# Performance work log

Hardware: AMD Instinct MI355X
Metric: run time of the kernel (lower is better)

Reference implementation:

```python
import jax, jax.numpy as jnp
import numpy as np
from jax import lax

BS, T, H, V, E, NREG, SEQ = 1024, 10, 256, 50000, 50, 1, 50
EPS = 1e-5


def _edge_index(bs):
    # get_batch_graph(max_len=10, windows=3): per graph, edges[0:-1] of combinations keeps
    # (j-3, j-2) and (j-3, j-1) for j in 3..10, plus (8,9) and (9,0). 18 edges/graph.
    e = []
    for j in range(3, 11):
        e += [(j - 3, j - 2), (j - 3, j - 1)]
    e += [(8, 9), (9, 0)]
    e = np.asarray(e, dtype=np.int32)                      # [18, 2]
    e = (e[None] + 10 * np.arange(bs, dtype=np.int32)[:, None, None]).reshape(-1, 2)
    return jnp.asarray(e[:, 0]), jnp.asarray(e[:, 1])      # src, dst


def setup_inputs() -> dict:
    key = jax.random.key(0)
    ks = jax.random.split(key, 24)
    s = 0.02
    inp = {
        'lags': jax.random.normal(ks[0], (BS, T), jnp.float32),
        'weather': jax.random.normal(ks[1], (BS, T, 2), jnp.float32),
        'event': jax.random.normal(ks[2], (BS, T, 4), jnp.float32),
        'text': jax.random.randint(ks[3], (BS, T, SEQ), 0, V, jnp.int32),
        'emb': jax.random.normal(ks[4], (V, E), jnp.float32) * s,
        'conv3_w': jax.random.normal(ks[5], (H // 2, E, 3), jnp.float32) * s,
        'conv3_b': jnp.zeros((H // 2,), jnp.float32),
        'conv4_w': jax.random.normal(ks[6], (H // 2, H // 2, 4), jnp.float32) * s,
        'conv4_b': jnp.zeros((H // 2,), jnp.float32),
        'lags_w': jax.random.normal(ks[7], (H, 1), jnp.float32) * s,
        'lags_b': jnp.zeros((H,), jnp.float32),
        'weather_w': jax.random.normal(ks[8], (H, 2), jnp.float32) * s,
        'weather_b': jnp.zeros((H,), jnp.float32),
        'event_w': jax.random.normal(ks[9], (H, 4), jnp.float32) * s,
        'event_b': jnp.zeros((H,), jnp.float32),
        'text_w': jax.random.normal(ks[10], (H, H // 2), jnp.float32) * s,
        'text_b': jnp.zeros((H,), jnp.float32),
        'merge_w': jax.random.normal(ks[11], (H, 4 * H), jnp.float32) * s,
        'merge_b': jnp.zeros((H,), jnp.float32),
        'bn_gamma': jnp.ones((H,), jnp.float32),
        'bn_beta': jnp.zeros((H,), jnp.float32),
        'mh_w': jax.random.normal(ks[12], (H, H), jnp.float32) * s,
        'mh_b': jnp.zeros((H,), jnp.float32),
        'gru_wih': jax.random.normal(ks[13], (3 * H, H), jnp.float32) * s,
        'gru_whh': jax.random.normal(ks[14], (3 * H, H), jnp.float32) * s,
        'gru_bih': jnp.zeros((3 * H,), jnp.float32),
        'gru_bhh': jnp.zeros((3 * H,), jnp.float32),
        'reg_w': jax.random.normal(ks[15], (NREG, T * H), jnp.float32) * s,
        'reg_b': jnp.zeros((NREG,), jnp.float32),
    }
    return inp


def _conv1d(x, w, b):
    # x: [N, Cin, L], w: [Cout, Cin, K] (torch layout)
    y = lax.conv_general_dilated(x, w, (1,), 'VALID',
                                 dimension_numbers=('NCH', 'OIH', 'NCH'))
    return y + b[None, :, None]


def _forward(lags, weather, event, text, emb, conv3_w, conv3_b, conv4_w, conv4_b,
             lags_w, lags_b, weather_w, weather_b, event_w, event_b, text_w, text_b,
             merge_w, merge_b, bn_gamma, bn_beta, mh_w, mh_b,
             gru_wih, gru_whh, gru_bih, gru_bhh, reg_w, reg_b):
    bs = lags.shape[0]
    n = bs * T
    h = mh_w.shape[0]

    # per-node feature projections
    l = lags.reshape(-1, 1) @ lags_w.T + lags_b                       # [N, H]
    w = weather.reshape(-1, 2) @ weather_w.T + weather_b              # [N, H]
    ev = event.reshape(-1, 4) @ event_w.T + event_b                   # [N, H]

    # text CNN branch (dropout = identity, eval mode)
    tx = emb[text.reshape(-1, SEQ)]                                   # [N, 50, E]
    tx = jnp.transpose(tx, (0, 2, 1))                                 # [N, E, 50]
    c3 = jax.nn.relu(_conv1d(tx, conv3_w, conv3_b))                   # [N, H/2, 48]
    c4 = jax.nn.relu(_conv1d(c3, conv4_w, conv4_b))                   # [N, H/2, 45]
    tx = jnp.max(c4, axis=2)                                          # [N, H/2]
    tx = tx @ text_w.T + text_b                                       # [N, H]

    # message passing: sum mailbox per destination node (all nodes have in-deg >= 1)
    src, dst = _edge_index(bs)
    def agg(f):
        return jax.ops.segment_sum(f[src], dst, num_segments=n)
    hcat = jnp.concatenate([agg(l), agg(w), agg(ev), agg(tx)], axis=-1)  # [N, 4H]

    # fused linear -> relu -> batchnorm (batch stats) -> linear
    m = jax.nn.relu(hcat @ merge_w.T + merge_b)
    mu = jnp.mean(m, axis=0)
    var = jnp.var(m, axis=0)
    m = (m - mu) / jnp.sqrt(var + EPS) * bn_gamma + bn_beta
    m = m @ mh_w.T + mh_b                                             # [N, H]

    # GRU over the 10 lag steps
    hg = m.reshape(bs, T, h)
    def step(hprev, x_t):
        gi = x_t @ gru_wih.T + gru_bih
        gh = hprev @ gru_whh.T + gru_bhh
        r = jax.nn.sigmoid(gi[:, :h] + gh[:, :h])
        z = jax.nn.sigmoid(gi[:, h:2 * h] + gh[:, h:2 * h])
        nn_ = jnp.tanh(gi[:, 2 * h:] + r * gh[:, 2 * h:])
        hnew = (1.0 - z) * nn_ + z * hprev
        return hnew, hnew
    h0 = jnp.zeros((bs, h), m.dtype)
    _, outs = lax.scan(step, h0, jnp.transpose(hg, (1, 0, 2)))        # [T, bs, H]
    out = jnp.transpose(outs, (1, 0, 2)).reshape(bs, -1)              # [bs, T*H]
    return out @ reg_w.T + reg_b                                      # [bs, n_reg]


def reference(lags, weather, event, text, emb, conv3_w, conv3_b, conv4_w, conv4_b,
              lags_w, lags_b, weather_w, weather_b, event_w, event_b, text_w, text_b,
              merge_w, merge_b, bn_gamma, bn_beta, mh_w, mh_b,
              gru_wih, gru_whh, gru_bih, gru_bhh, reg_w, reg_b):
    return _forward(lags, weather, event, text, emb, conv3_w, conv3_b, conv4_w, conv4_b,
                    lags_w, lags_b, weather_w, weather_b, event_w, event_b, text_w, text_b,
                    merge_w, merge_b, bn_gamma, bn_beta, mh_w, mh_b,
                    gru_wih, gru_whh, gru_bih, gru_bhh, reg_w, reg_b)
```

## Files before the change

### kernel.cpp

```cpp
#include <hip/hip_runtime.h>
#include <math.h>


typedef unsigned short u16;
typedef __attribute__((ext_vector_type(8))) short short8v;
typedef __attribute__((ext_vector_type(4))) float float4v;
#define MFMA16 __builtin_amdgcn_mfma_f32_16x16x32_bf16

__device__ inline u16 f2bf(float f) {
  unsigned u = __float_as_uint(f);
  u += 0x7FFFu + ((u >> 16) & 1u);
  return (u16)(u >> 16);
}

__global__ __launch_bounds__(256) void k_zero(float* __restrict__ p, int n) {
  int i = blockIdx.x * 256 + threadIdx.x;
  if (i < n) p[i] = 0.f;
}

__global__ __launch_bounds__(256) void k_repb3(const float* __restrict__ w3,
                                               u16* __restrict__ w3b) {
  int i = blockIdx.x * 256 + threadIdx.x;
  if (i >= 24576) return;
  int j = i & 7, l = (i >> 3) & 63, nt = (i >> 9) & 7, kt = i >> 12;
  int k = kt * 32 + (l >> 4) * 8 + j;
  int c = nt * 16 + (l & 15);
  int kk = k >> 6, e = k & 63;
  float v = (e < 50) ? w3[c * 150 + e * 3 + kk] : 0.f;
  w3b[i] = f2bf(v);
}

__global__ __launch_bounds__(256) void k_repb4(const float* __restrict__ w4,
                                               u16* __restrict__ w4b) {
  int i = blockIdx.x * 256 + threadIdx.x;
  int j = i & 7, l = (i >> 3) & 63, nt = (i >> 9) & 7, kt = i >> 12;
  int k = kt * 32 + (l >> 4) * 8 + j;
  int c = nt * 16 + (l & 15);
  int kk = k >> 7, ci = k & 127;
  w4b[i] = f2bf(w4[c * 512 + ci * 4 + kk]);
}

__global__ __launch_bounds__(256) void k_repwhh(const float* __restrict__ whh,
                                                u16* __restrict__ whhb) {
  int i = blockIdx.x * 256 + threadIdx.x;
  int j = i & 7, l = (i >> 3) & 63, kt = (i >> 9) & 7, nt = i >> 12;
  int n = nt * 16 + (l & 15);
  int k = kt * 32 + (l >> 4) * 8 + j;
  whhb[i] = f2bf(whh[n * 256 + k]);
}

__global__ __launch_bounds__(256) void k_pcomb(const float* __restrict__ wih,
                                               const float* __restrict__ mh_w,
                                               const float* __restrict__ mh_b,
                                               const float* __restrict__ bih,
                                               float* __restrict__ Wcomb,
                                               float* __restrict__ b1) {
  int g0 = blockIdx.x * 8, t = threadIdx.x;
  float acc[8] = {0.f, 0.f, 0.f, 0.f, 0.f, 0.f, 0.f, 0.f};
  for (int j = 0; j < 256; ++j) {
    float wv = mh_w[j * 256 + t];
#pragma unroll
    for (int r = 0; r < 8; ++r) acc[r] += wih[(g0 + r) * 256 + j] * wv;
  }
#pragma unroll
  for (int r = 0; r < 8; ++r) Wcomb[(g0 + r) * 256 + t] = acc[r];
  __shared__ float red[4][8];
  float mb = mh_b[t];
#pragma unroll
  for (int r = 0; r < 8; ++r) {
    float v = wih[(g0 + r) * 256 + t] * mb;
    v += __shfl_down(v, 32); v += __shfl_down(v, 16); v += __shfl_down(v, 8);
    v += __shfl_down(v, 4);  v += __shfl_down(v, 2);  v += __shfl_down(v, 1);
    if ((t & 63) == 0) red[t >> 6][r] = v;
  }
  __syncthreads();
  if (t < 8) b1[g0 + t] = bih[g0 + t] + red[0][t] + red[1][t] + red[2][t] + red[3][t];
}

__global__ __launch_bounds__(256) void k_pmerge(const float* __restrict__ merge_w,
                                                const float* __restrict__ text_w,
                                                const float* __restrict__ lags_w,
                                                const float* __restrict__ weather_w,
                                                const float* __restrict__ event_w,
                                                const float* __restrict__ lags_b,
                                                const float* __restrict__ weather_b,
                                                const float* __restrict__ event_b,
                                                const float* __restrict__ text_b,
                                                float* __restrict__ MtxT,
                                                float* __restrict__ A_l,
                                                float* __restrict__ MwT,
                                                float* __restrict__ MeT,
                                                float* __restrict__ bias_deg) {
  int blk = blockIdx.x, t = threadIdx.x;
  if (blk < 128) {
    int c = blk;
    float acc = 0.f;
    for (int j = 0; j < 256; ++j)
      acc += merge_w[t * 1024 + 768 + j] * text_w[j * 128 + c];
    MtxT[c * 256 + t] = acc;
  } else {
    float a = 0.f, w0 = 0.f, w1 = 0.f, e0 = 0.f, e1 = 0.f, e2 = 0.f, e3 = 0.f, bd = 0.f;
    for (int j = 0; j < 256; ++j) {
      float m0 = merge_w[t * 1024 + j];
      float m1 = merge_w[t * 1024 + 256 + j];
      float m2 = merge_w[t * 1024 + 512 + j];
      float m3 = merge_w[t * 1024 + 768 + j];
      a  += m0 * lags_w[j];
      w0 += m1 * weather_w[j * 2 + 0];
      w1 += m1 * weather_w[j * 2 + 1];
      e0 += m2 * event_w[j * 4 + 0];
      e1 += m2 * event_w[j * 4 + 1];
      e2 += m2 * event_w[j * 4 + 2];
      e3 += m2 * event_w[j * 4 + 3];
      bd += m0 * lags_b[j] + m1 * weather_b[j] + m2 * event_b[j] + m3 * text_b[j];
    }
    A_l[t] = a;
    MwT[t] = w0; MwT[256 + t] = w1;
    MeT[t] = e0; MeT[256 + t] = e1; MeT[512 + t] = e2; MeT[768 + t] = e3;
    bias_deg[t] = bd;
  }
}


#define LOADB4(DST, SRC, KT)                                                   \
  _Pragma("unroll") for (int q = 0; q < 4; ++q)                                \
      DST[q] = *(const short8v*)&SRC[((((KT) * 8 + NB + q) * 64) + l) * 8];

#define AFRAG3(AF, KT) {                                                       \
    const int kk_ = (KT) >> 1;                                                 \
    const int eb_ = 4 * ((KT) & 1) + g;                                        \
    _Pragma("unroll") for (int mt = 0; mt < 3; ++mt) {                         \
      int pr_ = 16 * mt + lr + kk_;                                            \
      int bb_ = eb_ ^ (pr_ & 7);                                               \
      AF[mt] = *(const short8v*)&sx[pr_ * 64 + bb_ * 8];                       \
    } }

#define AFRAG4(AF, KT) {                                                       \
    const int t4_ = 4 * (KT) + g;                                              \
    const int kk_ = t4_ >> 4;                                                  \
    const int bk_ = t4_ & 15;                                                  \
    _Pragma("unroll") for (int mt = 0; mt < 3; ++mt) {                         \
      int pr_ = 16 * mt + lr + kk_;                                            \
      int bb_ = (bk_ & 8) | ((bk_ ^ pr_) & 7);                                 \
      AF[mt] = *(const short8v*)&sc3[pr_ * 128 + bb_ * 8];                     \
    } }

#define MSTEP4(AF, BF)                                                         \
  _Pragma("unroll") for (int q = 0; q < 4; ++q)                                \
    _Pragma("unroll") for (int mt = 0; mt < 3; ++mt)                           \
      acc[mt][q] = MFMA16(AF[mt], BF[q], acc[mt][q], 0, 0, 0);

__global__ __launch_bounds__(128) void k_textcnn(const int* __restrict__ text,
                                                 const float* __restrict__ emb,
                                                 const u16* __restrict__ w3b,
                                                 const float* __restrict__ b3,
                                                 const u16* __restrict__ w4b,
                                                 const float* __restrict__ b4,
                                                 float* __restrict__ mx_g) {
  __shared__ u16 sbuf[52 * 128];
  u16* sx = sbuf;
  u16* sc3 = sbuf;
  const int n = blockIdx.x;
  const int t = threadIdx.x;
  const int wv = t >> 6;
  const int l = t & 63;
  const int lr = l & 15;
  const int g = l >> 4;
  const int NB = wv * 4;

  int idxv = (l < 25) ? text[n * 50 + wv * 25 + l] : 0;
  const int e = l;
#pragma unroll 5
  for (int si = 0; si < 25; ++si) {
    int s = wv * 25 + si;
    int id = __shfl(idxv, si);
    float v = (e < 50) ? emb[id * 50 + e] : 0.f;
    int bb = (e >> 3) ^ (s & 7);
    sx[s * 64 + bb * 8 + (e & 7)] = f2bf(v);
  }
  __syncthreads();

  const float4v zv = {0.f, 0.f, 0.f, 0.f};
  float4v acc[3][4];
#pragma unroll
  for (int mt = 0; mt < 3; ++mt)
#pragma unroll
    for (int q = 0; q < 4; ++q) acc[mt][q] = zv;

  float b3v[4];
#pragma unroll
  for (int q = 0; q < 4; ++q) b3v[q] = b3[(NB + q) * 16 + lr];

  {
    short8v bA[4], bB[4], a[3];
    LOADB4(bA, w3b, 0);
    for (int kt = 0; kt < 6; kt += 2) {
      LOADB4(bB, w3b, kt + 1);
      AFRAG3(a, kt);
      MSTEP4(a, bA);
      if (kt + 2 < 6) LOADB4(bA, w3b, kt + 2);
      AFRAG3(a, kt + 1);
      MSTEP4(a, bB);
    }
  }
  __syncthreads();

#pragma unroll
  for (int mt = 0; mt < 3; ++mt)
#pragma unroll
    for (int q = 0; q < 4; ++q) {
#pragma unroll
      for (int r = 0; r < 4; ++r) {
        int p = 16 * mt + 4 * g + r;
        int c = (NB + q) * 16 + lr;
        float v = fmaxf(acc[mt][q][r] + b3v[q], 0.f);
        int bb = (c >> 3) & 15;
        bb = (bb & 8) | ((bb ^ (p & 7)) & 7);
        sc3[p * 128 + bb * 8 + (c & 7)] = f2bf(v);
      }
      acc[mt][q] = zv;
    }
  __syncthreads();

  {
    short8v bA[4], bB[4], a[3];
    LOADB4(bA, w4b, 0);
    for (int kt = 0; kt < 16; kt += 2) {
      LOADB4(bB, w4b, kt + 1);
      AFRAG4(a, kt);
      MSTEP4(a, bA);
      if (kt + 2 < 16) LOADB4(bA, w4b, kt + 2);
      AFRAG4(a, kt + 1);
      MSTEP4(a, bB);
    }
  }

#pragma unroll
  for (int q = 0; q < 4; ++q) {
    float m0 = -1e30f;
#pragma unroll
    for (int mt = 0; mt < 3; ++mt)
#pragma unroll
      for (int r = 0; r < 4; ++r) {
        int p = 16 * mt + 4 * g + r;
        if (p < 45) m0 = fmaxf(m0, acc[mt][q][r]);
      }
    m0 = fmaxf(m0, __shfl_xor(m0, 16));
    m0 = fmaxf(m0, __shfl_xor(m0, 32));
    int c = (NB + q) * 16 + lr;
    float bias = b4[c];
    if (g == 0) mx_g[n * 128 + c] = fmaxf(m0 + bias, 0.f);
  }
}

__device__ inline void preds_of(int i, int& p1, int& p2, int& d) {
  int tt = i % 10;
  int base = i - tt;
  if (tt == 0)      { p1 = base + 9;      p2 = -1;             d = 1; }
  else if (tt == 1) { p1 = base;          p2 = -1;             d = 1; }
  else              { p1 = base + tt - 2; p2 = base + tt - 1;  d = 2; }
}

__global__ __launch_bounds__(256) void k_merge(const float* __restrict__ mx_g,
                                               const float* __restrict__ lags,
                                               const float* __restrict__ weather,
                                               const float* __restrict__ event,
                                               const float* __restrict__ MtxT,
                                               const float* __restrict__ A_l,
                                               const float* __restrict__ MwT,
                                               const float* __restrict__ MeT,
                                               const float* __restrict__ bias_deg,
                                               const float* __restrict__ merge_b,
                                               u16* __restrict__ m_bf,
                                               float* __restrict__ bnsum,
                                               float* __restrict__ bnsumsq) {
  __shared__ __align__(16) float mxs[16 * 128];
  __shared__ float scal[16 * 8];
  const int tid = threadIdx.x;
  const int row0 = blockIdx.x * 16;
  for (int idx = tid; idx < 2048; idx += 256) {
    int r = idx >> 7, c = idx & 127;
    int p1, p2, d;
    preds_of(row0 + r, p1, p2, d);
    float v = mx_g[p1 * 128 + c];
    if (p2 >= 0) v += mx_g[p2 * 128 + c];
    mxs[r * 128 + c] = v;
  }
  if (tid < 16) {
    int p1, p2, d;
    preds_of(row0 + tid, p1, p2, d);
    float sl = lags[p1];
    float sw0 = weather[p1 * 2], sw1 = weather[p1 * 2 + 1];
    float se0 = event[p1 * 4], se1 = event[p1 * 4 + 1];
    float se2 = event[p1 * 4 + 2], se3 = event[p1 * 4 + 3];
    if (p2 >= 0) {
      sl += lags[p2];
      sw0 += weather[p2 * 2]; sw1 += weather[p2 * 2 + 1];
      se0 += event[p2 * 4];     se1 += event[p2 * 4 + 1];
      se2 += event[p2 * 4 + 2]; se3 += event[p2 * 4 + 3];
    }
    scal[tid * 8 + 0] = sl;
    scal[tid * 8 + 1] = sw0; scal[tid * 8 + 2] = sw1;
    scal[tid * 8 + 3] = se0; scal[tid * 8 + 4] = se1;
    scal[tid * 8 + 5] = se2; scal[tid * 8 + 6] = se3;
    scal[tid * 8 + 7] = (float)d;
  }
  __syncthreads();
  const int t = tid;
  float acc[16];
#pragma unroll
  for (int r = 0; r < 16; ++r) acc[r] = 0.f;
  for (int c4 = 0; c4 < 32; ++c4) {
    const int c = c4 * 4;
    float w0 = MtxT[c * 256 + t];
    float w1 = MtxT[(c + 1) * 256 + t];
    float w2 = MtxT[(c + 2) * 256 + t];
    float w3 = MtxT[(c + 3) * 256 + t];
#pragma unroll
    for (int r = 0; r < 16; ++r) {
      float4 mv = *(const float4*)&mxs[r * 128 + c];
      acc[r] += mv.x * w0 + mv.y * w1 + mv.z * w2 + mv.w * w3;
    }
  }
  float al = A_l[t], mw0 = MwT[t], mw1 = MwT[256 + t];
  float me0 = MeT[t], me1 = MeT[256 + t], me2 = MeT[512 + t], me3 = MeT[768 + t];
  float bd = bias_deg[t], mb = merge_b[t];
  float s1 = 0.f, s2 = 0.f;
#pragma unroll
  for (int r = 0; r < 16; ++r) {
    float mp = acc[r] + scal[r * 8] * al + scal[r * 8 + 1] * mw0 + scal[r * 8 + 2] * mw1
             + scal[r * 8 + 3] * me0 + scal[r * 8 + 4] * me1 + scal[r * 8 + 5] * me2
             + scal[r * 8 + 6] * me3 + scal[r * 8 + 7] * bd + mb;
    float mv = fmaxf(mp, 0.f);
    m_bf[(row0 + r) * 256 + t] = f2bf(mv);
    s1 += mv;
    s2 += mv * mv;
  }
  atomicAdd(&bnsum[t], s1);
  atomicAdd(&bnsumsq[t], s2);
}

__global__ __launch_bounds__(256) void k_bna(const float* __restrict__ bnsum,
                                             const float* __restrict__ bnsumsq,
                                             const float* __restrict__ gamma,
                                             const float* __restrict__ beta,
                                             float* __restrict__ svec,
                                             float* __restrict__ tvec) {
  int c = threadIdx.x;
  float mu = bnsum[c] * (1.f / 10240.f);
  float var = bnsumsq[c] * (1.f / 10240.f) - mu * mu;
  float s = gamma[c] * rsqrtf(var + 1e-5f);
  svec[c] = s;
  tvec[c] = beta[c] - mu * s;
}

__global__ __launch_bounds__(256) void k_bnbc(const float* __restrict__ Wcomb,
                                              const float* __restrict__ svec,
                                              const float* __restrict__ tvec,
                                              const float* __restrict__ b1,
                                              u16* __restrict__ wbig_b,
                                              float* __restrict__ bias_big) {
  int blk = blockIdx.x, t = threadIdx.x;
  __shared__ float red[4];
  if (blk < 768) {
    int i = blk * 256 + t;
    int j = i & 7, l = (i >> 3) & 63, kt = (i >> 9) & 7, nt = i >> 12;
    int n = nt * 16 + (l & 15);
    int k = kt * 32 + (l >> 4) * 8 + j;
    wbig_b[i] = f2bf(Wcomb[n * 256 + k] * svec[k]);
  } else {
    int gg = blk - 768;
    float part = tvec[t] * Wcomb[gg * 256 + t];
    part += __shfl_down(part, 32); part += __shfl_down(part, 16);
    part += __shfl_down(part, 8);  part += __shfl_down(part, 4);
    part += __shfl_down(part, 2);  part += __shfl_down(part, 1);
    if ((t & 63) == 0) red[t >> 6] = part;
    __syncthreads();
    if (t == 0) bias_big[gg] = b1[gg] + red[0] + red[1] + red[2] + red[3];
  }
}

__global__ __launch_bounds__(256) void k_gi(const u16* __restrict__ m_bf,
                                            const u16* __restrict__ wbig_b,
                                            const float* __restrict__ bias_big,
                                            float* __restrict__ gi) {
  const int t = threadIdx.x;
  const int w = t >> 6, l = t & 63, lr = l & 15, g = l >> 4;
  const int row0 = blockIdx.x * 16;
  short8v a[8];
#pragma unroll
  for (int kt = 0; kt < 8; ++kt)
    a[kt] = *(const short8v*)&m_bf[(row0 + lr) * 256 + kt * 32 + g * 8];
  const float4v zv = {0.f, 0.f, 0.f, 0.f};
  float4v acc[12];
#pragma unroll
  for (int j = 0; j < 12; ++j) acc[j] = zv;
#pragma unroll 2
  for (int kt = 0; kt < 8; ++kt) {
#pragma unroll
    for (int j = 0; j < 12; ++j) {
      int nt = w * 12 + j;
      short8v b = *(const short8v*)&wbig_b[((nt * 8 + kt) * 64 + l) * 8];
      acc[j] = MFMA16(a[kt], b, acc[j], 0, 0, 0);
    }
  }
#pragma unroll
  for (int j = 0; j < 12; ++j) {
    int col = (w * 12 + j) * 16 + lr;
    float bb = bias_big[col];
#pragma unroll
    for (int r = 0; r < 4; ++r)
      gi[(row0 + g * 4 + r) * 768 + col] = acc[j][r] + bb;
  }
}

__global__ __launch_bounds__(512) void k_gru_all(const float* __restrict__ gi,
                                                 const u16* __restrict__ whhb,
                                                 const float* __restrict__ bhh,
                                                 const float* __restrict__ reg_w,
                                                 const float* __restrict__ reg_b,
                                                 float* __restrict__ out) {
  __shared__ u16 hb[16 * 256];
  __shared__ float red[8][16];
  const int t = threadIdx.x;
  const int w = t >> 6, l = t & 63, lr = l & 15, g = l >> 4;
  const int row0 = blockIdx.x * 16;
  for (int i = t; i < 4096; i += 512) hb[i] = 0;
  float hp[2][4];
#pragma unroll
  for (int i = 0; i < 2; ++i)
#pragma unroll
    for (int r = 0; r < 4; ++r) hp[i][r] = 0.f;
  float bh[3][2];
#pragma unroll
  for (int gate = 0; gate < 3; ++gate)
#pragma unroll
    for (int i = 0; i < 2; ++i)
      bh[gate][i] = bhh[gate * 256 + (2 * w + i) * 16 + lr];
  float racc[4] = {0.f, 0.f, 0.f, 0.f};

  for (int s = 0; s < 10; ++s) {
    __syncthreads();
    const float4v zv = {0.f, 0.f, 0.f, 0.f};
    float4v acc[3][2];
#pragma unroll
    for (int gate = 0; gate < 3; ++gate)
#pragma unroll
      for (int i = 0; i < 2; ++i) acc[gate][i] = zv;
#pragma unroll
    for (int kt = 0; kt < 8; ++kt) {
      int kb = kt * 4 + g;
      int bb = kb ^ (lr & 7);
      short8v a = *(const short8v*)&hb[lr * 256 + bb * 8];
#pragma unroll
      for (int gate = 0; gate < 3; ++gate)
#pragma unroll
        for (int i = 0; i < 2; ++i) {
          int nt = gate * 16 + 2 * w + i;
          short8v b = *(const short8v*)&whhb[((nt * 8 + kt) * 64 + l) * 8];
          acc[gate][i] = MFMA16(a, b, acc[gate][i], 0, 0, 0);
        }
    }
    __syncthreads();
#pragma unroll
    for (int i = 0; i < 2; ++i) {
      int c = (2 * w + i) * 16 + lr;
      float rwv = reg_w[s * 256 + c];
#pragma unroll
      for (int r = 0; r < 4; ++r) {
        int node = (row0 + g * 4 + r) * 10 + s;
        float gir = gi[node * 768 + c];
        float giz = gi[node * 768 + 256 + c];
        float gin = gi[node * 768 + 512 + c];
        float ghr = acc[0][i][r] + bh[0][i];
        float ghz = acc[1][i][r] + bh[1][i];
        float ghn = acc[2][i][r] + bh[2][i];
        float rg = 1.f / (1.f + expf(-(gir + ghr)));
        float zg = 1.f / (1.f + expf(-(giz + ghz)));
        float ng = tanhf(gin + rg * ghn);
        float hn = (1.f - zg) * ng + zg * hp[i][r];
        hp[i][r] = hn;
        racc[r] += hn * rwv;
        int m = g * 4 + r;
        int bb2 = (c >> 3) ^ (m & 7);
        hb[m * 256 + bb2 * 8 + (c & 7)] = f2bf(hn);
      }
    }
  }
#pragma unroll
  for (int r = 0; r < 4; ++r) {
    float v = racc[r];
    v += __shfl_xor(v, 1); v += __shfl_xor(v, 2);
    v += __shfl_xor(v, 4); v += __shfl_xor(v, 8);
    racc[r] = v;
  }
  if (lr == 0) {
#pragma unroll
    for (int r = 0; r < 4; ++r) red[w][g * 4 + r] = racc[r];
  }
  __syncthreads();
  if (t < 16) {
    float sum = reg_b[0];
#pragma unroll
    for (int w8 = 0; w8 < 8; ++w8) sum += red[w8][t];
    out[row0 + t] = sum;
  }
}

extern "C" void kernel_launch(void* const* d_in, const int* in_sizes, int n_in,
                              void* d_out, int out_size, void* d_ws, size_t ws_size,
                              hipStream_t stream) {
  (void)in_sizes; (void)n_in; (void)out_size; (void)ws_size;
  const float* lags      = (const float*)d_in[0];
  const float* weather   = (const float*)d_in[1];
  const float* event     = (const float*)d_in[2];
  const int*   text      = (const int*)d_in[3];
  const float* emb       = (const float*)d_in[4];
  const float* conv3_w   = (const float*)d_in[5];
  const float* conv3_b   = (const float*)d_in[6];
  const float* conv4_w   = (const float*)d_in[7];
  const float* conv4_b   = (const float*)d_in[8];
  const float* lags_w    = (const float*)d_in[9];
  const float* lags_b    = (const float*)d_in[10];
  const float* weather_w = (const float*)d_in[11];
  const float* weather_b = (const float*)d_in[12];
  const float* event_w   = (const float*)d_in[13];
  const float* event_b   = (const float*)d_in[14];
  const float* text_w    = (const float*)d_in[15];
  const float* text_b    = (const float*)d_in[16];
  const float* merge_w   = (const float*)d_in[17];
  const float* merge_b   = (const float*)d_in[18];
  const float* bn_gamma  = (const float*)d_in[19];
  const float* bn_beta   = (const float*)d_in[20];
  const float* mh_w      = (const float*)d_in[21];
  const float* mh_b      = (const float*)d_in[22];
  const float* gru_wih   = (const float*)d_in[23];
  const float* gru_whh   = (const float*)d_in[24];
  const float* gru_bih   = (const float*)d_in[25];
  const float* gru_bhh   = (const float*)d_in[26];
  const float* reg_w     = (const float*)d_in[27];
  const float* reg_b     = (const float*)d_in[28];
  float* out = (float*)d_out;

  float* p = (float*)d_ws;
  float* bnsum    = p; p += 256;
  float* bnsumsq  = p; p += 256;
  float* mx       = p; p += 10240 * 128;
  u16*   m_bf     = (u16*)p; p += 10240 * 128;
  float* gi       = p; p += 10240 * 768;
  u16*   w3b      = (u16*)p; p += 12288;
  u16*   w4b      = (u16*)p; p += 32768;
  u16*   whhb     = (u16*)p; p += 98304;
  u16*   wbig_b   = (u16*)p; p += 98304;
  float* Wcomb    = p; p += 196608;
  float* MtxT     = p; p += 32768;
  float* A_l      = p; p += 256;
  float* MwT      = p; p += 512;
  float* MeT      = p; p += 1024;
  float* bias_deg = p; p += 256;
  float* b1       = p; p += 768;
  float* bias_big = p; p += 768;
  float* svec     = p; p += 256;
  float* tvec     = p; p += 256;

  k_zero<<<dim3(2), dim3(256), 0, stream>>>(bnsum, 512);
  k_repb3<<<dim3(96), dim3(256), 0, stream>>>(conv3_w, w3b);
  k_repb4<<<dim3(256), dim3(256), 0, stream>>>(conv4_w, w4b);
  k_repwhh<<<dim3(768), dim3(256), 0, stream>>>(gru_whh, whhb);
  k_pcomb<<<dim3(96), dim3(256), 0, stream>>>(gru_wih, mh_w, mh_b, gru_bih, Wcomb, b1);
  k_pmerge<<<dim3(129), dim3(256), 0, stream>>>(merge_w, text_w, lags_w, weather_w, event_w,
                                                lags_b, weather_b, event_b, text_b,
                                                MtxT, A_l, MwT, MeT, bias_deg);
  k_textcnn<<<dim3(10240), dim3(128), 0, stream>>>(text, emb, w3b, conv3_b, w4b, conv4_b, mx);
  k_merge<<<dim3(640), dim3(256), 0, stream>>>(mx, lags, weather, event, MtxT, A_l, MwT, MeT,
                                               bias_deg, merge_b, m_bf, bnsum, bnsumsq);
  k_bna<<<dim3(1), dim3(256), 0, stream>>>(bnsum, bnsumsq, bn_gamma, bn_beta, svec, tvec);
  k_bnbc<<<dim3(1536), dim3(256), 0, stream>>>(Wcomb, svec, tvec, b1, wbig_b, bias_big);
  k_gi<<<dim3(640), dim3(256), 0, stream>>>(m_bf, wbig_b, bias_big, gi);
  k_gru_all<<<dim3(64), dim3(512), 0, stream>>>(gi, whhb, gru_bhh, reg_w, reg_b, out);
}
```

Baseline: 564.6 us.

## Split textcnn across four waves and pre-transpose merge_w for coalesced reads

The text CNN kernel now runs with 256 threads (4 waves), each wave covering 2 output column tiles instead of 4. Embedding gather is spread over the four waves with a strided loop. This raises wave-level parallelism per block and halves per-wave accumulator registers, at the cost of more blocks' worth of threads sharing LDS and barriers. Separately, merge_w is transposed once into a scratch buffer (aliasing mx before textcnn writes it) so k_pmerge reads it with coalesced accesses.

```diff
diff --git a/kernel.cpp b/kernel.cpp
--- a/kernel.cpp
+++ b/kernel.cpp
@@ -49,6 +49,21 @@
   whhb[i] = f2bf(whh[n * 256 + k]);
 }
 
+__global__ __launch_bounds__(256) void k_tr(const float* __restrict__ A,
+                                            float* __restrict__ AT) {
+  __shared__ float tile[32][33];
+  int bx = blockIdx.x;
+  int by = blockIdx.y;
+  int lx = threadIdx.x & 31, ly = threadIdx.x >> 5;
+#pragma unroll
+  for (int i = 0; i < 4; ++i)
+    tile[ly + i * 8][lx] = A[(by * 32 + ly + i * 8) * 1024 + bx * 32 + lx];
+  __syncthreads();
+#pragma unroll
+  for (int i = 0; i < 4; ++i)
+    AT[(bx * 32 + ly + i * 8) * 256 + by * 32 + lx] = tile[lx][ly + i * 8];
+}
+
 __global__ __launch_bounds__(256) void k_pcomb(const float* __restrict__ wih,
                                                const float* __restrict__ mh_w,
                                                const float* __restrict__ mh_b,
@@ -77,7 +92,7 @@
   if (t < 8) b1[g0 + t] = bih[g0 + t] + red[0][t] + red[1][t] + red[2][t] + red[3][t];
 }
 
-__global__ __launch_bounds__(256) void k_pmerge(const float* __restrict__ merge_w,
+__global__ __launch_bounds__(256) void k_pmerge(const float* __restrict__ mwT,
                                                 const float* __restrict__ text_w,
                                                 const float* __restrict__ lags_w,
                                                 const float* __restrict__ weather_w,
@@ -96,15 +111,15 @@
     int c = blk;
     float acc = 0.f;
     for (int j = 0; j < 256; ++j)
-      acc += merge_w[t * 1024 + 768 + j] * text_w[j * 128 + c];
+      acc += mwT[(768 + j) * 256 + t] * text_w[j * 128 + c];
     MtxT[c * 256 + t] = acc;
   } else {
     float a = 0.f, w0 = 0.f, w1 = 0.f, e0 = 0.f, e1 = 0.f, e2 = 0.f, e3 = 0.f, bd = 0.f;
     for (int j = 0; j < 256; ++j) {
-      float m0 = merge_w[t * 1024 + j];
-      float m1 = merge_w[t * 1024 + 256 + j];
-      float m2 = merge_w[t * 1024 + 512 + j];
-      float m3 = merge_w[t * 1024 + 768 + j];
+      float m0 = mwT[j * 256 + t];
+      float m1 = mwT[(256 + j) * 256 + t];
+      float m2 = mwT[(512 + j) * 256 + t];
+      float m3 = mwT[(768 + j) * 256 + t];
       a  += m0 * lags_w[j];
       w0 += m1 * weather_w[j * 2 + 0];
       w1 += m1 * weather_w[j * 2 + 1];
@@ -122,8 +137,8 @@
 }
 
 
-#define LOADB4(DST, SRC, KT)                                                   \
-  _Pragma("unroll") for (int q = 0; q < 4; ++q)                                \
+#define LOADB2(DST, SRC, KT)                                                   \
+  _Pragma("unroll") for (int q = 0; q < 2; ++q)                                \
       DST[q] = *(const short8v*)&SRC[((((KT) * 8 + NB + q) * 64) + l) * 8];
 
 #define AFRAG3(AF, KT) {                                                       \
@@ -145,12 +160,12 @@
       AF[mt] = *(const short8v*)&sc3[pr_ * 128 + bb_ * 8];                     \
     } }
 
-#define MSTEP4(AF, BF)                                                         \
-  _Pragma("unroll") for (int q = 0; q < 4; ++q)                                \
+#define MSTEP2(AF, BF)                                                         \
+  _Pragma("unroll") for (int q = 0; q < 2; ++q)                                \
     _Pragma("unroll") for (int mt = 0; mt < 3; ++mt)                           \
       acc[mt][q] = MFMA16(AF[mt], BF[q], acc[mt][q], 0, 0, 0);
 
-__global__ __launch_bounds__(128) void k_textcnn(const int* __restrict__ text,
+__global__ __launch_bounds__(256) void k_textcnn(const int* __restrict__ text,
                                                  const float* __restrict__ emb,
                                                  const u16* __restrict__ w3b,
                                                  const float* __restrict__ b3,
@@ -166,14 +181,12 @@
   const int l = t & 63;
   const int lr = l & 15;
   const int g = l >> 4;
-  const int NB = wv * 4;
-
-  int idxv = (l < 25) ? text[n * 50 + wv * 25 + l] : 0;
+  const int NB = wv * 2;
+
+  int idxv = (l < 50) ? text[n * 50 + l] : 0;
   const int e = l;
-#pragma unroll 5
-  for (int si = 0; si < 25; ++si) {
-    int s = wv * 25 + si;
-    int id = __shfl(idxv, si);
+  for (int s = wv; s < 50; s += 4) {
+    int id = __shfl(idxv, s);
     float v = (e < 50) ? emb[id * 50 + e] : 0.f;
     int bb = (e >> 3) ^ (s & 7);
     sx[s * 64 + bb * 8 + (e & 7)] = f2bf(v);
@@ -181,26 +194,26 @@
   __syncthreads();
 
   const float4v zv = {0.f, 0.f, 0.f, 0.f};
-  float4v acc[3][4];
+  float4v acc[3][2];
 #pragma unroll
   for (int mt = 0; mt < 3; ++mt)
 #pragma unroll
-    for (int q = 0; q < 4; ++q) acc[mt][q] = zv;
-
-  float b3v[4];
-#pragma unroll
-  for (int q = 0; q < 4; ++q) b3v[q] = b3[(NB + q) * 16 + lr];
+    for (int q = 0; q < 2; ++q) acc[mt][q] = zv;
+
+  float b3v[2];
+#pragma unroll
+  for (int q = 0; q < 2; ++q) b3v[q] = b3[(NB + q) * 16 + lr];
 
   {
-    short8v bA[4], bB[4], a[3];
-    LOADB4(bA, w3b, 0);
+    short8v bA[2], bB[2], a[3];
+    LOADB2(bA, w3b, 0);
     for (int kt = 0; kt < 6; kt += 2) {
-      LOADB4(bB, w3b, kt + 1);
+      LOADB2(bB, w3b, kt + 1);
       AFRAG3(a, kt);
-      MSTEP4(a, bA);
-      if (kt + 2 < 6) LOADB4(bA, w3b, kt + 2);
+      MSTEP2(a, bA);
+      if (kt + 2 < 6) LOADB2(bA, w3b, kt + 2);
       AFRAG3(a, kt + 1);
-      MSTEP4(a, bB);
+      MSTEP2(a, bB);
     }
   }
   __syncthreads();
@@ -208,7 +221,7 @@
 #pragma unroll
   for (int mt = 0; mt < 3; ++mt)
 #pragma unroll
-    for (int q = 0; q < 4; ++q) {
+    for (int q = 0; q < 2; ++q) {
 #pragma unroll
       for (int r = 0; r < 4; ++r) {
         int p = 16 * mt + 4 * g + r;
@@ -223,20 +236,20 @@
   __syncthreads();
 
   {
-    short8v bA[4], bB[4], a[3];
-    LOADB4(bA, w4b, 0);
+    short8v bA[2], bB[2], a[3];
+    LOADB2(bA, w4b, 0);
     for (int kt = 0; kt < 16; kt += 2) {
-      LOADB4(bB, w4b, kt + 1);
+      LOADB2(bB, w4b, kt + 1);
       AFRAG4(a, kt);
-      MSTEP4(a, bA);
-      if (kt + 2 < 16) LOADB4(bA, w4b, kt + 2);
+      MSTEP2(a, bA);
+      if (kt + 2 < 16) LOADB2(bA, w4b, kt + 2);
       AFRAG4(a, kt + 1);
-      MSTEP4(a, bB);
-    }
-  }
-
-#pragma unroll
-  for (int q = 0; q < 4; ++q) {
+      MSTEP2(a, bB);
+    }
+  }
+
+#pragma unroll
+  for (int q = 0; q < 2; ++q) {
     float m0 = -1e30f;
 #pragma unroll
     for (int mt = 0; mt < 3; ++mt)
@@ -562,16 +575,18 @@
   float* bias_big = p; p += 768;
   float* svec     = p; p += 256;
   float* tvec     = p; p += 256;
+  float* mwT      = mx;
 
   k_zero<<<dim3(2), dim3(256), 0, stream>>>(bnsum, 512);
   k_repb3<<<dim3(96), dim3(256), 0, stream>>>(conv3_w, w3b);
   k_repb4<<<dim3(256), dim3(256), 0, stream>>>(conv4_w, w4b);
   k_repwhh<<<dim3(768), dim3(256), 0, stream>>>(gru_whh, whhb);
+  k_tr<<<dim3(32, 8), dim3(256), 0, stream>>>(merge_w, mwT);
   k_pcomb<<<dim3(96), dim3(256), 0, stream>>>(gru_wih, mh_w, mh_b, gru_bih, Wcomb, b1);
-  k_pmerge<<<dim3(129), dim3(256), 0, stream>>>(merge_w, text_w, lags_w, weather_w, event_w,
+  k_pmerge<<<dim3(129), dim3(256), 0, stream>>>(mwT, text_w, lags_w, weather_w, event_w,
                                                 lags_b, weather_b, event_b, text_b,
                                                 MtxT, A_l, MwT, MeT, bias_deg);
-  k_textcnn<<<dim3(10240), dim3(128), 0, stream>>>(text, emb, w3b, conv3_b, w4b, conv4_b, mx);
+  k_textcnn<<<dim3(10240), dim3(256), 0, stream>>>(text, emb, w3b, conv3_b, w4b, conv4_b, mx);
   k_merge<<<dim3(640), dim3(256), 0, stream>>>(mx, lags, weather, event, MtxT, A_l, MwT, MeT,
                                                bias_deg, merge_b, m_bf, bnsum, bnsumsq);
   k_bna<<<dim3(1), dim3(256), 0, stream>>>(bnsum, bnsumsq, bn_gamma, bn_beta, svec, tvec);
```

Measured after the change: 544.3 us. -3.6%, faster.
